# Kernel tuning notes

Hardware: AMD Instinct MI355X
Metric: run time of the kernel (lower is better)

Reference implementation:

```python
import jax, jax.numpy as jnp
import numpy as np

N = 2_097_152  # total atoms
G = 32_768     # number of graphs (~64 atoms each)
EPS = 1e-4     # sign-detection threshold from the original code


def setup_inputs() -> dict:
    key = jax.random.key(0)
    k1, k2 = jax.random.split(key)
    pos = jax.random.normal(k1, (N, 3), dtype=jnp.float32) * 3.0
    batch = jnp.sort(jax.random.randint(k2, (N,), 0, G))
    return {"pos": pos, "batch": batch, "num_graphs": G}


def reference(pos, batch, num_graphs):
    n = pos.shape[0]
    dtype = pos.dtype

    # per-graph centroid (scatter_mean)
    counts = jax.ops.segment_sum(jnp.ones((n,), dtype), batch, num_segments=num_graphs)
    center = jax.ops.segment_sum(pos, batch, num_segments=num_graphs) / jnp.maximum(counts, 1.0)[:, None]
    pc = pos - center[batch]                      # [N,3] centered positions

    # per-atom inertia contribution: r^2 * I - p p^T, then scatter_add per graph
    r_sq = jnp.sum(pc * pc, axis=-1)              # [N]
    outer = jnp.einsum('ni,nj->nij', pc, pc)      # [N,3,3]
    I_atom = r_sq[:, None, None] * jnp.eye(3, dtype=dtype) - outer
    I_mol = jax.ops.segment_sum(I_atom, batch, num_segments=num_graphs)  # [G,3,3]

    L, Q = jnp.linalg.eigh(I_mol)                 # Q: [G,3,3], columns = principal axes

    # projections of centered positions onto the (pre-flip) eigenbasis.
    # NOTE: in the torch loop, p_proj is computed once before any sign flips, and
    # flipping column 0 does not affect p_proj[:,1], so axes 0 and 1 are independent.
    proj = jnp.einsum('ni,nij->nj', pc, Q[batch])  # [N,3]

    idx = jnp.arange(n)

    def axis_sign(a):
        # parallel "first atom (in original order) with |proj| > EPS" per graph
        qual = jnp.abs(proj[:, a]) > EPS
        key_idx = jnp.where(qual, idx, n)
        first = jax.ops.segment_min(key_idx, batch, num_segments=num_graphs)  # [G]
        found = first < n
        val = proj[jnp.minimum(first, n - 1), a]
        return jnp.where(found & (val < 0), -1.0, 1.0).astype(dtype)

    s0 = axis_sign(0)
    s1 = axis_sign(1)
    q0 = Q[:, :, 0] * s0[:, None]
    q1 = Q[:, :, 1] * s1[:, None]
    q2 = jnp.cross(q0, q1)  # enforce right-handed frame
    return jnp.stack([q0, q1, q2], axis=-1)       # [G,3,3]
```

## Files before the change

kernel.cpp:

```cpp
#include <hip/hip_runtime.h>
#include <math.h>

#define CANON_EPS 1e-4f

__global__ __launch_bounds__(256) void build_starts_kernel(
    const int* __restrict__ batch, int* __restrict__ wsi, int n, int G) {
  int i = (int)(blockIdx.x * (unsigned)blockDim.x + threadIdx.x);
  if (i >= n) return;
  int b = batch[i];
  int bp = (i == 0) ? -1 : batch[i - 1];
  for (int g = bp + 1; g <= b; ++g) wsi[g] = i;
  if (i == n - 1) {
    for (int g = b + 1; g <= G; ++g) wsi[G > g ? g : G] = n;
  }
}

__global__ __launch_bounds__(256) void moments_kernel(
    const float* __restrict__ pos, const int* __restrict__ wsi,
    float* __restrict__ wsf, int G) {
  int tid = (int)(blockIdx.x * (unsigned)blockDim.x + threadIdx.x);
  int gid = tid >> 4;
  int sub = tid & 15;
  if (gid >= G) return;

  int s = wsi[gid];
  int e = wsi[gid + 1];
  int cnt = e - s;

  float sx = 0.f, sy = 0.f, sz = 0.f;
  float sxx = 0.f, syy = 0.f, szz = 0.f, sxy = 0.f, sxz = 0.f, syz = 0.f;

#pragma unroll
  for (int k = 0; k < 5; ++k) {
    int i = s + sub + 16 * k;
    bool in = i < e;
    int ii = in ? i : s;
    float m = in ? 1.0f : 0.0f;
    float x = pos[3 * ii + 0] * m;
    float y = pos[3 * ii + 1] * m;
    float z = pos[3 * ii + 2] * m;
    sx += x; sy += y; sz += z;
    sxx = fmaf(x, x, sxx); syy = fmaf(y, y, syy); szz = fmaf(z, z, szz);
    sxy = fmaf(x, y, sxy); sxz = fmaf(x, z, sxz); syz = fmaf(y, z, syz);
  }
  for (int i = s + 80 + sub; i < e; i += 16) {
    float x = pos[3 * i + 0];
    float y = pos[3 * i + 1];
    float z = pos[3 * i + 2];
    sx += x; sy += y; sz += z;
    sxx = fmaf(x, x, sxx); syy = fmaf(y, y, syy); szz = fmaf(z, z, szz);
    sxy = fmaf(x, y, sxy); sxz = fmaf(x, z, sxz); syz = fmaf(y, z, syz);
  }

#define RED16(v)                                                             \
  v += __shfl_xor(v, 1); v += __shfl_xor(v, 2);                              \
  v += __shfl_xor(v, 4); v += __shfl_xor(v, 8);
  RED16(sx) RED16(sy) RED16(sz)
  RED16(sxx) RED16(syy) RED16(szz)
  RED16(sxy) RED16(sxz) RED16(syz)
#undef RED16

  float fn = (float)(cnt > 0 ? cnt : 1);
  float inv = 1.0f / fn;
  float mx = sx * inv, my = sy * inv, mz = sz * inv;
  float Sxx = fmaf(-fn * mx, mx, sxx);
  float Syy = fmaf(-fn * my, my, syy);
  float Szz = fmaf(-fn * mz, mz, szz);
  float Sxy = fmaf(-fn * mx, my, sxy);
  float Sxz = fmaf(-fn * mx, mz, sxz);
  float Syz = fmaf(-fn * my, mz, syz);

  float v = mx;
  v = (sub == 1) ? my : v;
  v = (sub == 2) ? mz : v;
  v = (sub == 3) ? (Syy + Szz) : v;
  v = (sub == 4) ? (Sxx + Szz) : v;
  v = (sub == 5) ? (Sxx + Syy) : v;
  v = (sub == 6) ? (-Sxy) : v;
  v = (sub == 7) ? (-Sxz) : v;
  if (sub < 8) wsf[sub * G + gid] = v;
  if (sub == 0) wsf[8 * G + gid] = -Syz;
}

__device__ __forceinline__ void jacobi3_f32(float a00, float a11, float a22,
                                            float a01, float a02, float a12,
                                            float Q[3][3]) {
  float A00 = a00, A11 = a11, A22 = a22;
  float A01 = a01, A02 = a02, A12 = a12;
  float Q00 = 1.f, Q01 = 0.f, Q02 = 0.f;
  float Q10 = 0.f, Q11 = 1.f, Q12 = 0.f;
  float Q20 = 0.f, Q21 = 0.f, Q22 = 1.f;

#define ROT(App, Aqq, Apq, Akp, Akq, Qrp0, Qrq0, Qrp1, Qrq1, Qrp2, Qrq2)     \
  {                                                                          \
    float apq = Apq;                                                         \
    float theta = (Aqq - App) / (2.0f * apq);                                \
    float t = copysignf(1.0f, theta) /                                       \
              (fabsf(theta) + sqrtf(1.0f + theta * theta));                  \
    t = (apq == 0.0f) ? 0.0f : t;                    \
    float c = 1.0f / sqrtf(1.0f + t * t);                                    \
    float s = t * c;                                                         \
    App = App - t * apq;                                                     \
    Aqq = Aqq + t * apq;                                                     \
    Apq = 0.0f;                                                              \
    float akp = Akp, akq = Akq;                                              \
    Akp = c * akp - s * akq;                                                 \
    Akq = s * akp + c * akq;                                                 \
    float r0p = Qrp0, r0q = Qrq0;                                            \
    Qrp0 = c * r0p - s * r0q;                                                \
    Qrq0 = s * r0p + c * r0q;                                                \
    float r1p = Qrp1, r1q = Qrq1;                                            \
    Qrp1 = c * r1p - s * r1q;                                                \
    Qrq1 = s * r1p + c * r1q;                                                \
    float r2p = Qrp2, r2q = Qrq2;                                            \
    Qrp2 = c * r2p - s * r2q;                                                \
    Qrq2 = s * r2p + c * r2q;                                                \
  }

#pragma unroll
  for (int sweep = 0; sweep < 5; ++sweep) {
    ROT(A00, A11, A01, A02, A12, Q00, Q01, Q10, Q11, Q20, Q21);
    ROT(A00, A22, A02, A01, A12, Q00, Q02, Q10, Q12, Q20, Q22);
    ROT(A11, A22, A12, A01, A02, Q01, Q02, Q11, Q12, Q21, Q22);
  }
#undef ROT

  float w0 = A00, w1 = A11, w2 = A22;
#define CSWAP(wa, wb, qa0, qb0, qa1, qb1, qa2, qb2)                          \
  {                                                                          \
    bool sw = (wb) < (wa);                                                   \
    float tw = wa; wa = sw ? wb : wa; wb = sw ? tw : wb;                     \
    float t0 = qa0; qa0 = sw ? qb0 : qa0; qb0 = sw ? t0 : qb0;               \
    float t1 = qa1; qa1 = sw ? qb1 : qa1; qb1 = sw ? t1 : qb1;               \
    float t2 = qa2; qa2 = sw ? qb2 : qa2; qb2 = sw ? t2 : qb2;               \
  }
  CSWAP(w0, w1, Q00, Q01, Q10, Q11, Q20, Q21);
  CSWAP(w1, w2, Q01, Q02, Q11, Q12, Q21, Q22);
  CSWAP(w0, w1, Q00, Q01, Q10, Q11, Q20, Q21);
#undef CSWAP

  Q[0][0] = Q00; Q[0][1] = Q01; Q[0][2] = Q02;
  Q[1][0] = Q10; Q[1][1] = Q11; Q[1][2] = Q12;
  Q[2][0] = Q20; Q[2][1] = Q21; Q[2][2] = Q22;
}

__global__ __launch_bounds__(256) void eigen_kernel(
    const float* __restrict__ pos, const int* __restrict__ wsi,
    const float* __restrict__ wsf, float* __restrict__ out, int G) {
  int g = (int)(blockIdx.x * (unsigned)blockDim.x + threadIdx.x);
  if (g >= G) return;

  int s = wsi[g];
  int e = wsi[g + 1];

  float cx  = wsf[0 * G + g];
  float cy  = wsf[1 * G + g];
  float cz  = wsf[2 * G + g];
  float ixx = wsf[3 * G + g];
  float iyy = wsf[4 * G + g];
  float izz = wsf[5 * G + g];
  float ixy = wsf[6 * G + g];
  float ixz = wsf[7 * G + g];
  float iyz = wsf[8 * G + g];

  float Q[3][3];
  jacobi3_f32(ixx, iyy, izz, ixy, ixz, iyz, Q);

  float q00 = Q[0][0], q10 = Q[1][0], q20 = Q[2][0];
  float q01 = Q[0][1], q11 = Q[1][1], q21 = Q[2][1];

  bool found0 = false, found1 = false;
  float v0 = 0.f, v1 = 0.f;
  for (int base = s; base < e && !(found0 && found1); base += 4) {
    float px[4], py[4], pz[4];
    bool iv[4];
#pragma unroll
    for (int j = 0; j < 4; ++j) {
      int i = base + j;
      bool in = i < e;
      iv[j] = in;
      int ii = in ? i : s;
      px[j] = pos[3 * ii + 0];
      py[j] = pos[3 * ii + 1];
      pz[j] = pos[3 * ii + 2];
    }
#pragma unroll
    for (int j = 0; j < 4; ++j) {
      if (iv[j]) {
        float x = px[j] - cx, y = py[j] - cy, z = pz[j] - cz;
        float p0 = x * q00 + y * q10 + z * q20;
        float p1 = x * q01 + y * q11 + z * q21;
        if (!found0 && fabsf(p0) > CANON_EPS) { v0 = p0; found0 = true; }
        if (!found1 && fabsf(p1) > CANON_EPS) { v1 = p1; found1 = true; }
      }
    }
  }
  float s0 = (found0 && v0 < 0.f) ? -1.f : 1.f;
  float s1 = (found1 && v1 < 0.f) ? -1.f : 1.f;

  float q0x = q00 * s0, q0y = q10 * s0, q0z = q20 * s0;
  float q1x = q01 * s1, q1y = q11 * s1, q1z = q21 * s1;
  float q2x = q0y * q1z - q0z * q1y;
  float q2y = q0z * q1x - q0x * q1z;
  float q2z = q0x * q1y - q0y * q1x;
  float* o = out + (size_t)g * 9;
  o[0] = q0x; o[1] = q1x; o[2] = q2x;
  o[3] = q0y; o[4] = q1y; o[5] = q2y;
  o[6] = q0z; o[7] = q1z; o[8] = q2z;
}

extern "C" void kernel_launch(void* const* d_in, const int* in_sizes, int n_in,
                              void* d_out, int out_size, void* d_ws, size_t ws_size,
                              hipStream_t stream) {
  const float* pos = (const float*)d_in[0];
  const int* batch = (const int*)d_in[1];
  float* out = (float*)d_out;

  int n = in_sizes[0] / 3;
  int G = out_size / 9;

  int* wsi = (int*)d_ws;
  float* wsf = (float*)((char*)d_ws + (((size_t)(G + 1) * 4 + 255) & ~255ull));

  build_starts_kernel<<<(n + 255) / 256, 256, 0, stream>>>(batch, wsi, n, G);

  moments_kernel<<<(G * 16 + 255) / 256, 256, 0, stream>>>(pos, wsi, wsf, G);

  eigen_kernel<<<(G + 255) / 256, 256, 0, stream>>>(pos, wsi, wsf, out, G);
}
```

Before: 22.73 us.

## Vectorize segment-start scan, interleave moment layout, prefetch first atoms, trim Jacobi sweeps

The segment-start kernel now has each thread read four batch entries with an int4 load, cutting the thread count. The moments workspace moves from structure-of-arrays to nine contiguous floats per graph, and the eigen kernel reads it that way. The eigen kernel issues loads for its first four atoms before the Jacobi solve so their latency overlaps the math, uses 64-thread blocks, and drops one Jacobi sweep. Other edits are a clamp-index tweak and an odd `szz*0.f` term in the tail loop. Fewer sweeps may cost eigenvector accuracy in near-degenerate cases.

New measurement: 21.42 us. -5.8%, faster.

```diff
diff --git a/kernel.cpp b/kernel.cpp
--- a/kernel.cpp
+++ b/kernel.cpp
@@ -5,13 +5,33 @@
 
 __global__ __launch_bounds__(256) void build_starts_kernel(
     const int* __restrict__ batch, int* __restrict__ wsi, int n, int G) {
-  int i = (int)(blockIdx.x * (unsigned)blockDim.x + threadIdx.x);
-  if (i >= n) return;
-  int b = batch[i];
-  int bp = (i == 0) ? -1 : batch[i - 1];
-  for (int g = bp + 1; g <= b; ++g) wsi[g] = i;
-  if (i == n - 1) {
-    for (int g = b + 1; g <= G; ++g) wsi[G > g ? g : G] = n;
+  int t = (int)(blockIdx.x * (unsigned)blockDim.x + threadIdx.x);
+  int base = t * 4;
+  if (base >= n) return;
+
+  int b0, b1, b2, b3;
+  if (base + 4 <= n) {
+    int4 b4 = *reinterpret_cast<const int4*>(batch + base);
+    b0 = b4.x; b1 = b4.y; b2 = b4.z; b3 = b4.w;
+  } else {
+    b0 = batch[base];
+    b1 = (base + 1 < n) ? batch[base + 1] : b0;
+    b2 = (base + 2 < n) ? batch[base + 2] : b1;
+    b3 = (base + 3 < n) ? batch[base + 3] : b2;
+  }
+  int bp = (base > 0) ? batch[base - 1] : -1;
+
+  int B[4] = {b0, b1, b2, b3};
+#pragma unroll
+  for (int j = 0; j < 4; ++j) {
+    int i = base + j;
+    if (i >= n) break;
+    int prev = (j == 0) ? bp : B[j - 1];
+    int b = B[j];
+    for (int g = prev + 1; g <= b; ++g) wsi[g] = i;
+    if (i == n - 1) {
+      for (int g = b + 1; g <= G; ++g) wsi[g] = n;
+    }
   }
 }
 
@@ -34,7 +54,7 @@
   for (int k = 0; k < 5; ++k) {
     int i = s + sub + 16 * k;
     bool in = i < e;
-    int ii = in ? i : s;
+    int ii = in ? i : 0;
     float m = in ? 1.0f : 0.0f;
     float x = pos[3 * ii + 0] * m;
     float y = pos[3 * ii + 1] * m;
@@ -48,7 +68,7 @@
     float y = pos[3 * i + 1];
     float z = pos[3 * i + 2];
     sx += x; sy += y; sz += z;
-    sxx = fmaf(x, x, sxx); syy = fmaf(y, y, syy); szz = fmaf(z, z, szz);
+    sxx = fmaf(x, x, sxx); syy = fmaf(y, y, szz * 0.f + syy); szz = fmaf(z, z, szz);
     sxy = fmaf(x, y, sxy); sxz = fmaf(x, z, sxz); syz = fmaf(y, z, syz);
   }
 
@@ -78,8 +98,8 @@
   v = (sub == 5) ? (Sxx + Syy) : v;
   v = (sub == 6) ? (-Sxy) : v;
   v = (sub == 7) ? (-Sxz) : v;
-  if (sub < 8) wsf[sub * G + gid] = v;
-  if (sub == 0) wsf[8 * G + gid] = -Syz;
+  v = (sub == 8) ? (-Syz) : v;
+  if (sub < 9) wsf[(size_t)gid * 9 + sub] = v;
 }
 
 __device__ __forceinline__ void jacobi3_f32(float a00, float a11, float a22,
@@ -118,7 +138,7 @@
   }
 
 #pragma unroll
-  for (int sweep = 0; sweep < 5; ++sweep) {
+  for (int sweep = 0; sweep < 4; ++sweep) {
     ROT(A00, A11, A01, A02, A12, Q00, Q01, Q10, Q11, Q20, Q21);
     ROT(A00, A22, A02, A01, A12, Q00, Q02, Q10, Q12, Q20, Q22);
     ROT(A11, A22, A12, A01, A02, Q01, Q02, Q11, Q12, Q21, Q22);
@@ -144,7 +164,7 @@
   Q[2][0] = Q20; Q[2][1] = Q21; Q[2][2] = Q22;
 }
 
-__global__ __launch_bounds__(256) void eigen_kernel(
+__global__ __launch_bounds__(64) void eigen_kernel(
     const float* __restrict__ pos, const int* __restrict__ wsi,
     const float* __restrict__ wsf, float* __restrict__ out, int G) {
   int g = (int)(blockIdx.x * (unsigned)blockDim.x + threadIdx.x);
@@ -153,15 +173,28 @@
   int s = wsi[g];
   int e = wsi[g + 1];
 
-  float cx  = wsf[0 * G + g];
-  float cy  = wsf[1 * G + g];
-  float cz  = wsf[2 * G + g];
-  float ixx = wsf[3 * G + g];
-  float iyy = wsf[4 * G + g];
-  float izz = wsf[5 * G + g];
-  float ixy = wsf[6 * G + g];
-  float ixz = wsf[7 * G + g];
-  float iyz = wsf[8 * G + g];
+  const float* m = wsf + (size_t)g * 9;
+  float cx  = m[0];
+  float cy  = m[1];
+  float cz  = m[2];
+  float ixx = m[3];
+  float iyy = m[4];
+  float izz = m[5];
+  float ixy = m[6];
+  float ixz = m[7];
+  float iyz = m[8];
+
+  float px0, py0, pz0, px1, py1, pz1, px2, py2, pz2, px3, py3, pz3;
+  {
+    int i0 = (s + 0 < e) ? s + 0 : 0;
+    int i1 = (s + 1 < e) ? s + 1 : 0;
+    int i2 = (s + 2 < e) ? s + 2 : 0;
+    int i3 = (s + 3 < e) ? s + 3 : 0;
+    px0 = pos[3 * i0 + 0]; py0 = pos[3 * i0 + 1]; pz0 = pos[3 * i0 + 2];
+    px1 = pos[3 * i1 + 0]; py1 = pos[3 * i1 + 1]; pz1 = pos[3 * i1 + 2];
+    px2 = pos[3 * i2 + 0]; py2 = pos[3 * i2 + 1]; pz2 = pos[3 * i2 + 2];
+    px3 = pos[3 * i3 + 0]; py3 = pos[3 * i3 + 1]; pz3 = pos[3 * i3 + 2];
+  }
 
   float Q[3][3];
   jacobi3_f32(ixx, iyy, izz, ixy, ixz, iyz, Q);
@@ -171,29 +204,27 @@
 
   bool found0 = false, found1 = false;
   float v0 = 0.f, v1 = 0.f;
-  for (int base = s; base < e && !(found0 && found1); base += 4) {
-    float px[4], py[4], pz[4];
-    bool iv[4];
-#pragma unroll
-    for (int j = 0; j < 4; ++j) {
-      int i = base + j;
-      bool in = i < e;
-      iv[j] = in;
-      int ii = in ? i : s;
-      px[j] = pos[3 * ii + 0];
-      py[j] = pos[3 * ii + 1];
-      pz[j] = pos[3 * ii + 2];
-    }
-#pragma unroll
-    for (int j = 0; j < 4; ++j) {
-      if (iv[j]) {
-        float x = px[j] - cx, y = py[j] - cy, z = pz[j] - cz;
-        float p0 = x * q00 + y * q10 + z * q20;
-        float p1 = x * q01 + y * q11 + z * q21;
-        if (!found0 && fabsf(p0) > CANON_EPS) { v0 = p0; found0 = true; }
-        if (!found1 && fabsf(p1) > CANON_EPS) { v1 = p1; found1 = true; }
-      }
-    }
+#define CHECK(PX, PY, PZ, J)                                                 \
+  if (s + (J) < e) {                                                         \
+    float x = (PX) - cx, y = (PY) - cy, z = (PZ) - cz;                       \
+    float p0 = x * q00 + y * q10 + z * q20;                                  \
+    float p1 = x * q01 + y * q11 + z * q21;                                  \
+    if (!found0 && fabsf(p0) > CANON_EPS) { v0 = p0; found0 = true; }        \
+    if (!found1 && fabsf(p1) > CANON_EPS) { v1 = p1; found1 = true; }        \
+  }
+  CHECK(px0, py0, pz0, 0)
+  CHECK(px1, py1, pz1, 1)
+  CHECK(px2, py2, pz2, 2)
+  CHECK(px3, py3, pz3, 3)
+#undef CHECK
+  for (int i = s + 4; i < e && !(found0 && found1); ++i) {
+    float x = pos[3 * i + 0] - cx;
+    float y = pos[3 * i + 1] - cy;
+    float z = pos[3 * i + 2] - cz;
+    float p0 = x * q00 + y * q10 + z * q20;
+    float p1 = x * q01 + y * q11 + z * q21;
+    if (!found0 && fabsf(p0) > CANON_EPS) { v0 = p0; found0 = true; }
+    if (!found1 && fabsf(p1) > CANON_EPS) { v1 = p1; found1 = true; }
   }
   float s0 = (found0 && v0 < 0.f) ? -1.f : 1.f;
   float s1 = (found1 && v1 < 0.f) ? -1.f : 1.f;
@@ -222,9 +253,10 @@
   int* wsi = (int*)d_ws;
   float* wsf = (float*)((char*)d_ws + (((size_t)(G + 1) * 4 + 255) & ~255ull));
 
-  build_starts_kernel<<<(n + 255) / 256, 256, 0, stream>>>(batch, wsi, n, G);
+  int t1 = (n + 3) / 4;
+  build_starts_kernel<<<(t1 + 255) / 256, 256, 0, stream>>>(batch, wsi, n, G);
 
   moments_kernel<<<(G * 16 + 255) / 256, 256, 0, stream>>>(pos, wsi, wsf, G);
 
-  eigen_kernel<<<(G + 255) / 256, 256, 0, stream>>>(pos, wsi, wsf, out, G);
-}
+  eigen_kernel<<<(G + 63) / 64, 64, 0, stream>>>(pos, wsi, wsf, out, G);
+}
```
